# Kernel tuning notes

Measured on AMD Instinct MI355X. Metric: run time of the kernel, lower is better.

## Reference

```python
import jax, jax.numpy as jnp
import numpy as np

HIDDEN = 2048
NUM_HEADS = 16
HEAD_DIM = 128
KV_C = 512
Q_C = 1536
ROPE_DIM = 64
B, S = 2, 2048


def _rope(x):
    # x: [B, H, S, D] with D even; interleaved-pair rotation as in the torch module
    b, h, s, d = x.shape
    inv_freq = 1.0 / (10000.0 ** (jnp.arange(0, d, 2, dtype=jnp.float32) / d))  # [d/2]
    pos = jnp.arange(s, dtype=jnp.float32)
    sinusoid = pos[:, None] * inv_freq[None, :]  # [S, d/2]
    sin, cos = jnp.sin(sinusoid), jnp.cos(sinusoid)
    xr = x.reshape(b, h, s, d // 2, 2)
    x1, x2 = xr[..., 0], xr[..., 1]
    out = jnp.stack([x1 * cos - x2 * sin, x1 * sin + x2 * cos], axis=-1)
    return out.reshape(b, h, s, d)


def setup_inputs() -> dict:
    key = jax.random.key(0)
    ks = jax.random.split(key, 12)

    def lin(k, fan_in, fan_out):
        k1, k2 = jax.random.split(k)
        lim = 1.0 / np.sqrt(fan_in)
        w = jax.random.uniform(k1, (fan_in, fan_out), jnp.float32, -lim, lim)
        b = jax.random.uniform(k2, (fan_out,), jnp.float32, -lim, lim)
        return w, b

    kv_down_w, kv_down_b = lin(ks[0], HIDDEN, KV_C)
    key_up_w, key_up_b = lin(ks[1], KV_C, NUM_HEADS * HEAD_DIM)
    value_up_w, value_up_b = lin(ks[2], KV_C, NUM_HEADS * HEAD_DIM)
    key_rope_w, key_rope_b = lin(ks[3], KV_C, NUM_HEADS * ROPE_DIM)
    query_down_w, query_down_b = lin(ks[4], HIDDEN, Q_C)
    query_up_w, query_up_b = lin(ks[5], Q_C, NUM_HEADS * HEAD_DIM)
    query_rope_w, query_rope_b = lin(ks[6], Q_C, NUM_HEADS * ROPE_DIM)
    out_w, out_b = lin(ks[7], NUM_HEADS * HEAD_DIM, HIDDEN)

    x = jax.random.normal(ks[8], (B, S, HIDDEN), jnp.float32)
    attention_mask = jnp.ones((B, S), dtype=jnp.bool_)  # all tokens valid

    return dict(x=x, attention_mask=attention_mask,
                kv_down_w=kv_down_w, kv_down_b=kv_down_b,
                key_up_w=key_up_w, key_up_b=key_up_b,
                value_up_w=value_up_w, value_up_b=value_up_b,
                key_rope_w=key_rope_w, key_rope_b=key_rope_b,
                query_down_w=query_down_w, query_down_b=query_down_b,
                query_up_w=query_up_w, query_up_b=query_up_b,
                query_rope_w=query_rope_w, query_rope_b=query_rope_b,
                out_w=out_w, out_b=out_b)


def reference(x, attention_mask,
              kv_down_w, kv_down_b, key_up_w, key_up_b,
              value_up_w, value_up_b, key_rope_w, key_rope_b,
              query_down_w, query_down_b, query_up_w, query_up_b,
              query_rope_w, query_rope_b, out_w, out_b):
    b, s, _ = x.shape

    kv_c = x @ kv_down_w + kv_down_b                                 # [B,S,KV_C]
    keys_c = (kv_c @ key_up_w + key_up_b).reshape(b, s, NUM_HEADS, HEAD_DIM).transpose(0, 2, 1, 3)
    values = (kv_c @ value_up_w + value_up_b).reshape(b, s, NUM_HEADS, HEAD_DIM).transpose(0, 2, 1, 3)
    keys_r = (kv_c @ key_rope_w + key_rope_b).reshape(b, s, NUM_HEADS, ROPE_DIM).transpose(0, 2, 1, 3)
    keys_r = _rope(keys_r)

    q_c = x @ query_down_w + query_down_b                            # [B,S,Q_C]
    queries_c = (q_c @ query_up_w + query_up_b).reshape(b, s, NUM_HEADS, HEAD_DIM).transpose(0, 2, 1, 3)
    queries_r = (q_c @ query_rope_w + query_rope_b).reshape(b, s, NUM_HEADS, ROPE_DIM).transpose(0, 2, 1, 3)
    queries_r = _rope(queries_r)

    queries = jnp.concatenate([queries_c, queries_r], axis=-1)      # [B,H,S,HD+RD]
    keys = jnp.concatenate([keys_c, keys_r], axis=-1)

    scale = 1.0 / np.sqrt(HEAD_DIM + ROPE_DIM)
    scores = jnp.einsum('bhqd,bhkd->bhqk', queries, keys) * scale   # [B,H,S,S]

    causal = jnp.triu(jnp.ones((s, s), dtype=jnp.bool_), k=1)       # True = masked
    pad = ~attention_mask                                            # [B,S], True = masked key
    mask = causal[None, None, :, :] | pad[:, None, None, :]
    scores = jnp.where(mask, jnp.float32(-1e9), scores)

    probs = jax.nn.softmax(scores, axis=-1)
    context = jnp.einsum('bhqk,bhkd->bhqd', probs, values)          # [B,H,S,HD]
    context = context.transpose(0, 2, 1, 3).reshape(b, s, NUM_HEADS * HEAD_DIM)
    return context @ out_w + out_b                                   # [B,S,HIDDEN]
```

## Files before the change

kernel.cpp:

```cpp
#include <hip/hip_runtime.h>

typedef unsigned short u16;
typedef short short8 __attribute__((ext_vector_type(8)));
typedef short short4v __attribute__((ext_vector_type(4)));
typedef float floatx4 __attribute__((ext_vector_type(4)));
typedef float floatx4v __attribute__((ext_vector_type(4)));

#define SQ 2048
#define NH 16
#define HD 128
#define RD 64
#define NB 2
#define LDKV 5120
#define LDQ 3072

#define LKC 136
#define LKR 72
#define LVT 72
#define LP  72

#define OFF_BC   ((size_t)0)
#define OFF_WT1  ((size_t)16384)
#define OFF_WT2  (OFF_WT1 + (size_t)2048 * 2048)
#define OFF_WT3  (OFF_WT2 + (size_t)5120 * 512)
#define OFF_WTO  (OFF_WT3 + (size_t)3072 * 1536)
#define OFF_KVQD (OFF_WTO + (size_t)2048 * 2048)
#define OFF_KV   (OFF_KVQD + (size_t)4096 * 2048)
#define OFF_QB   (OFF_KV + (size_t)4096 * 5120)
#define OFF_ROPE (OFF_QB + (size_t)4096 * 3072)

__device__ __forceinline__ float bf2f(u16 u) {
  union { unsigned u; float f; } v; v.u = ((unsigned)u) << 16; return v.f;
}
__device__ __forceinline__ u16 f2bf(float f) {
  union { float f; unsigned u; } v; v.f = f;
  return (u16)((v.u + 0x7FFFu + ((v.u >> 16) & 1u)) >> 16);
}
__device__ __forceinline__ void gll16(const u16* g, u16* l) {
  __builtin_amdgcn_global_load_lds((const __attribute__((address_space(1))) void*)g,
                                   (__attribute__((address_space(3))) void*)l, 16, 0, 0);
}

__global__ __launch_bounds__(256) void prep(
    const float* __restrict__ x,
    const float* b0, const float* b1, const float* b2, const float* b3,
    const float* b4, const float* b5, const float* b6, const float* b7,
    const float* w0, const float* w1, const float* w2, const float* w3,
    const float* w4, const float* w5, const float* w6, const float* w7,
    u16* __restrict__ ws) {
  __shared__ u16 tile[32][33];
  const int blk = blockIdx.x, t = threadIdx.x;

  if (blk < 8192) {
    const int i = blk * 256 + t;
    const floatx4v v = *(const floatx4v*)(x + 4 * (size_t)i);
    short4v o;
    o.x = (short)f2bf(v.x); o.y = (short)f2bf(v.y);
    o.z = (short)f2bf(v.z); o.w = (short)f2bf(v.w);
    *(short4v*)(ws + OFF_QB + 4 * (size_t)i) = o;
    return;
  }
  if (blk < 8240) {
    const int i = (blk - 8192) * 256 + t;
    if (i >= 12288) return;
    float v;
    if      (i < 512)   v = b0[i];
    else if (i < 2048)  v = b1[i - 512];
    else if (i < 4096)  v = b2[i - 2048];
    else if (i < 6144)  v = b3[i - 4096];
    else if (i < 7168)  v = b4[i - 6144];
    else if (i < 9216)  v = b5[i - 7168];
    else if (i < 10240) v = b6[i - 9216];
    else                v = b7[i - 10240];
    ws[OFF_BC + i] = f2bf(v);
    return;
  }
  if (blk >= 23600) {
    const int i = (blk - 23600) * 256 + t;
    const int s = i >> 5, j = i & 31;
    const float inv = exp2f(-(float)j * 0.41524101186092031f);
    float sn, cs;
    sincosf((float)s * inv, &sn, &cs);
    float* rt = (float*)(ws + OFF_ROPE);
    rt[2 * i]     = cs;
    rt[2 * i + 1] = sn;
    return;
  }
  const int f = blk - 8240;
  const float* in; size_t oo; int R, C, start;
  if      (f < 1024)  { in = w0; oo = OFF_WT1;                        R = 2048; C = 512;  start = 0; }
  else if (f < 4096)  { in = w1; oo = OFF_WT1 + (size_t)512 * 2048;   R = 2048; C = 1536; start = 1024; }
  else if (f < 5120)  { in = w2; oo = OFF_WT2;                        R = 512;  C = 2048; start = 4096; }
  else if (f < 6144)  { in = w3; oo = OFF_WT2 + (size_t)2048 * 512;   R = 512;  C = 2048; start = 5120; }
  else if (f < 6656)  { in = w4; oo = OFF_WT2 + (size_t)4096 * 512;   R = 512;  C = 1024; start = 6144; }
  else if (f < 9728)  { in = w5; oo = OFF_WT3;                        R = 1536; C = 2048; start = 6656; }
  else if (f < 11264) { in = w6; oo = OFF_WT3 + (size_t)2048 * 1536;  R = 1536; C = 1024; start = 9728; }
  else                { in = w7; oo = OFF_WTO;                        R = 2048; C = 2048; start = 11264; }
  u16* out = ws + oo;
  const int local = f - start, nx = C / 32;
  const int c0 = (local % nx) * 32, r0 = (local / nx) * 32;
  const int xx = t & 31, y = t >> 5;
#pragma unroll
  for (int i = 0; i < 32; i += 8)
    tile[y + i][xx] = f2bf(in[(size_t)(r0 + y + i) * C + c0 + xx]);
  __syncthreads();
#pragma unroll
  for (int i = 0; i < 32; i += 8)
    out[(size_t)(c0 + y + i) * R + r0 + xx] = tile[xx][y + i];
}

__global__ __launch_bounds__(256) void post(u16* __restrict__ ws) {
  __shared__ u16 tile[32][33];
  const int blk = blockIdx.x, t = threadIdx.x;

  if (blk < 8192) {
    u16* buf = ws + OFF_KV;
    const float* rt = (const float*)(ws + OFF_ROPE);
    const int i = blk * 256 + t;
    const int j = i & 31;
    const int hh = (i >> 5) & 15;
    const int row = i >> 9;
    const int s = row & (SQ - 1);
    u16* p = buf + (size_t)row * LDKV + 4096 + hh * RD + 2 * j;
    const float2 t2 = *(const float2*)(rt + ((size_t)s * 32 + j) * 2);
    const float x1 = bf2f(p[0]), x2 = bf2f(p[1]);
    p[0] = f2bf(x1 * t2.x - x2 * t2.y);
    p[1] = f2bf(x1 * t2.y + x2 * t2.x);
    return;
  }
  const int f = blk - 8192;
  const int bh = f >> 8, rem = f & 255;
  const int b = bh >> 4, hh = bh & 15;
  const int s0 = (rem & 63) * 32, d0 = (rem >> 6) * 32;
  const u16* pin = ws + OFF_KV + (size_t)b * SQ * LDKV + 2048 + (size_t)hh * HD;
  u16* pout = ws + OFF_KVQD + (size_t)bh * HD * SQ;
  const int xx = t & 31, y = t >> 5;
#pragma unroll
  for (int i = 0; i < 32; i += 8)
    tile[y + i][xx] = pin[(size_t)(s0 + y + i) * LDKV + d0 + xx];
  __syncthreads();
#pragma unroll
  for (int i = 0; i < 32; i += 8)
    pout[(size_t)(d0 + y + i) * SQ + s0 + xx] = tile[xx][y + i];
}

__global__ __launch_bounds__(512, 4) void gemm_bt(
    int split,
    const u16* __restrict__ A1, int lda1, const u16* __restrict__ B1,
    const u16* __restrict__ bias1, void* __restrict__ C1, int ldc1, int wf1, int N1, int K1,
    const u16* __restrict__ A2, int lda2, const u16* __restrict__ B2,
    const u16* __restrict__ bias2, void* __restrict__ C2, int ldc2, int wf2, int N2, int K2) {
  __shared__ __align__(16) u16 lAk0[128 * 32];
  __shared__ __align__(16) u16 lAk1[128 * 32];
  __shared__ __align__(16) u16 lBk0[128 * 32];
  __shared__ __align__(16) u16 lBk1[128 * 32];
  int id = blockIdx.x;
  const u16 *A, *Bt, *bias; void* Cout; int lda, ldc, wf32, N, K;
  if (id < split) {
    A = A1; lda = lda1; Bt = B1; bias = bias1; Cout = C1; ldc = ldc1; wf32 = wf1; N = N1; K = K1;
  } else {
    id -= split;
    A = A2; lda = lda2; Bt = B2; bias = bias2; Cout = C2; ldc = ldc2; wf32 = wf2; N = N2; K = K2;
  }
  const int nx = N >> 7;
  const int m0 = (id / nx) * 128, n0 = (id % nx) * 128;
  const int t = threadIdx.x;
  const int lane = t & 63, w = t >> 6;
  const int wm = w & 1, wn = w >> 1;
  const int srow = t >> 2, scol = (t & 3) * 8;
  const u16* gA = A + (size_t)(m0 + srow) * lda + scol;
  const u16* gB = Bt + (size_t)(n0 + srow) * K + scol;
  u16* const ldA0 = lAk0 + (16 * w) * 32;
  u16* const ldA1 = lAk1 + (16 * w) * 32;
  u16* const ldB0 = lBk0 + (16 * w) * 32;
  u16* const ldB1 = lBk1 + (16 * w) * 32;
  const int lane_m = lane & 15, lane_k = (lane >> 4) * 8;
  floatx4 acc[4][2] = {};
  for (int k0 = 0; k0 < K; k0 += 64) {
    gll16(gA + k0, ldA0);
    gll16(gA + k0 + 32, ldA1);
    gll16(gB + k0, ldB0);
    gll16(gB + k0 + 32, ldB1);
    __syncthreads();
    {
      short8 af[4], bf[2];
#pragma unroll
      for (int i = 0; i < 4; i++)
        af[i] = *(const short8*)(lAk0 + (wm * 64 + i * 16 + lane_m) * 32 + lane_k);
#pragma unroll
      for (int i = 0; i < 2; i++)
        bf[i] = *(const short8*)(lBk0 + (wn * 32 + i * 16 + lane_m) * 32 + lane_k);
#pragma unroll
      for (int mi = 0; mi < 4; mi++)
#pragma unroll
        for (int ni = 0; ni < 2; ni++)
          acc[mi][ni] = __builtin_amdgcn_mfma_f32_16x16x32_bf16(af[mi], bf[ni], acc[mi][ni], 0, 0, 0);
    }
    {
      short8 af[4], bf[2];
#pragma unroll
      for (int i = 0; i < 4; i++)
        af[i] = *(const short8*)(lAk1 + (wm * 64 + i * 16 + lane_m) * 32 + lane_k);
#pragma unroll
      for (int i = 0; i < 2; i++)
        bf[i] = *(const short8*)(lBk1 + (wn * 32 + i * 16 + lane_m) * 32 + lane_k);
#pragma unroll
      for (int mi = 0; mi < 4; mi++)
#pragma unroll
        for (int ni = 0; ni < 2; ni++)
          acc[mi][ni] = __builtin_amdgcn_mfma_f32_16x16x32_bf16(af[mi], bf[ni], acc[mi][ni], 0, 0, 0);
    }
    __syncthreads();
  }
  const int quad = lane >> 4;
#pragma unroll
  for (int ni = 0; ni < 2; ni++) {
    const int col = n0 + wn * 32 + ni * 16 + lane_m;
    const float bv = bf2f(bias[col]);
#pragma unroll
    for (int mi = 0; mi < 4; mi++) {
      const int row = m0 + wm * 64 + mi * 16 + quad * 4;
      if (wf32) {
        float* pc = (float*)Cout + (size_t)row * ldc + col;
#pragma unroll
        for (int r = 0; r < 4; r++)
          pc[(size_t)r * ldc] = acc[mi][ni][r] + bv;
      } else {
        u16* pc = (u16*)Cout + (size_t)row * ldc + col;
#pragma unroll
        for (int r = 0; r < 4; r++)
          pc[(size_t)r * ldc] = f2bf(acc[mi][ni][r] + bv);
      }
    }
  }
}

__global__ __launch_bounds__(512, 4) void flash_attn(const u16* __restrict__ Q,
                                                     const u16* __restrict__ KV,
                                                     const u16* __restrict__ Vt,
                                                     const float* __restrict__ rt,
                                                     u16* __restrict__ Ctx) {
  __shared__ __align__(16) u16 lKc[64 * LKC];
  __shared__ __align__(16) u16 lKr[64 * LKR];
  __shared__ __align__(16) u16 lVt[128 * LVT];
  __shared__ __align__(16) u16 lP[8 * 16 * LP];
  const int t = threadIdx.x, lane = t & 63, w = t >> 6;
  const int col = blockIdx.y;
  const int qtile = (col < 16) ? (15 - (int)blockIdx.x) : (int)blockIdx.x;
  const int h = col & (NH - 1);
  const int b = col >> 4;
  const int q0 = qtile * 128;
  const int nkt = 2 * qtile + 2;
  const int lane_m = lane & 15, quad = lane >> 4, lane_k = quad * 8;

  const int qrow = q0 + 16 * w + lane_m;
  const u16* qcp = Q + (size_t)(b * SQ + qrow) * LDQ + h * HD;
  const u16* qrp = Q + (size_t)(b * SQ + qrow) * LDQ + 2048 + h * RD;
  short8 qfc[4], qfr[2];
#pragma unroll
  for (int ks = 0; ks < 4; ks++) qfc[ks] = *(const short8*)(qcp + ks * 32 + lane_k);
  {
#pragma unroll
    for (int ks = 0; ks < 2; ks++) {
      short8 v = *(const short8*)(qrp + ks * 32 + lane_k);
#pragma unroll
      for (int p = 0; p < 4; p++) {
        const int j = ks * 16 + quad * 4 + p;
        const float2 t2 = *(const float2*)(rt + ((size_t)qrow * 32 + j) * 2);
        const float x1 = bf2f((u16)v[2 * p]), x2 = bf2f((u16)v[2 * p + 1]);
        v[2 * p]     = (short)f2bf(x1 * t2.x - x2 * t2.y);
        v[2 * p + 1] = (short)f2bf(x1 * t2.y + x2 * t2.x);
      }
      qfr[ks] = v;
    }
  }

  floatx4 O[8] = {};
  float mrow[4], lsum[4];
#pragma unroll
  for (int r = 0; r < 4; r++) { mrow[r] = -1e30f; lsum[r] = 0.f; }

  const u16* gKc = KV + (size_t)b * SQ * LDKV + h * HD;
  const u16* gKr = KV + (size_t)b * SQ * LDKV + 4096 + h * RD;
  const u16* gVt = Vt + (size_t)(b * NH + h) * HD * SQ;
  const float C2 = 0.10412825525540364f;
  const float THR = 28.8f;

  short8 rKc[2], rKr, rVt[2];
  auto load_tile = [&](int kb) {
#pragma unroll
    for (int i = 0; i < 2; i++) {
      const int c = t + i * 512, row = c >> 4, cc = (c & 15) * 8;
      rKc[i] = *(const short8*)(gKc + (size_t)(kb + row) * LDKV + cc);
    }
    {
      const int row = t >> 3, cc = (t & 7) * 8;
      rKr = *(const short8*)(gKr + (size_t)(kb + row) * LDKV + cc);
    }
#pragma unroll
    for (int i = 0; i < 2; i++) {
      const int c = t + i * 512, row = c >> 3, cc = (c & 7) * 8;
      rVt[i] = *(const short8*)(gVt + (size_t)row * SQ + kb + cc);
    }
  };

  const int wrow_lo = q0 + 16 * w;
  const int wrow_hi = wrow_lo + 15;

  load_tile(0);
  for (int kt = 0; kt < nkt; kt++) {
    const int kb = kt * 64;
    __syncthreads();
#pragma unroll
    for (int i = 0; i < 2; i++) {
      const int c = t + i * 512, row = c >> 4, cc = (c & 15) * 8;
      *(short8*)(lKc + row * LKC + cc) = rKc[i];
    }
    {
      const int row = t >> 3, cc = (t & 7) * 8;
      *(short8*)(lKr + row * LKR + cc) = rKr;
    }
#pragma unroll
    for (int i = 0; i < 2; i++) {
      const int c = t + i * 512, row = c >> 3, cc = (c & 7) * 8;
      *(short8*)(lVt + row * LVT + cc) = rVt[i];
    }
    __syncthreads();
    if (kt < nkt - 1) load_tile(kb + 64);

    if (kb <= wrow_hi) {
      float ss[4][4];
      __builtin_amdgcn_s_setprio(1);
#pragma unroll
      for (int n = 0; n < 4; n++) {
        floatx4 a = {0.f, 0.f, 0.f, 0.f};
#pragma unroll
        for (int ks = 0; ks < 4; ks++) {
          const short8 kf = *(const short8*)(lKc + (n * 16 + lane_m) * LKC + ks * 32 + lane_k);
          a = __builtin_amdgcn_mfma_f32_16x16x32_bf16(qfc[ks], kf, a, 0, 0, 0);
        }
#pragma unroll
        for (int ks = 0; ks < 2; ks++) {
          const short8 kf = *(const short8*)(lKr + (n * 16 + lane_m) * LKR + ks * 32 + lane_k);
          a = __builtin_amdgcn_mfma_f32_16x16x32_bf16(qfr[ks], kf, a, 0, 0, 0);
        }
#pragma unroll
        for (int r = 0; r < 4; r++) ss[n][r] = a[r];
      }
      __builtin_amdgcn_s_setprio(0);
      if (kb + 63 > wrow_lo) {
#pragma unroll
        for (int n = 0; n < 4; n++) {
          const int kcol = kb + n * 16 + lane_m;
#pragma unroll
          for (int r = 0; r < 4; r++) {
            const int row = wrow_lo + quad * 4 + r;
            if (kcol > row) ss[n][r] = -1e30f;
          }
        }
      }
      float mt[4];
#pragma unroll
      for (int r = 0; r < 4; r++) {
        float m = fmaxf(fmaxf(ss[0][r], ss[1][r]), fmaxf(ss[2][r], ss[3][r]));
#pragma unroll
        for (int d = 1; d < 16; d <<= 1) m = fmaxf(m, __shfl_xor(m, d));
        mt[r] = m;
      }
      const bool grow = (mt[0] > mrow[0] + THR) || (mt[1] > mrow[1] + THR) ||
                        (mt[2] > mrow[2] + THR) || (mt[3] > mrow[3] + THR);
      if (__any(grow)) {
#pragma unroll
        for (int r = 0; r < 4; r++) {
          const float mn = fmaxf(mrow[r], mt[r]);
          const float alpha = exp2f((mrow[r] - mn) * C2);
          mrow[r] = mn;
          lsum[r] *= alpha;
#pragma unroll
          for (int vb = 0; vb < 8; vb++) O[vb][r] *= alpha;
        }
      }
      float pw[4][4];
#pragma unroll
      for (int r = 0; r < 4; r++) {
        float s = 0.f;
#pragma unroll
        for (int n = 0; n < 4; n++) {
          const float p = exp2f((ss[n][r] - mrow[r]) * C2);
          pw[n][r] = p;
          s += p;
        }
#pragma unroll
        for (int d = 1; d < 16; d <<= 1) s += __shfl_xor(s, d);
        lsum[r] += s;
      }
#pragma unroll
      for (int n = 0; n < 4; n++)
#pragma unroll
        for (int r = 0; r < 4; r++)
          lP[(w * 16 + quad * 4 + r) * LP + n * 16 + lane_m] = f2bf(pw[n][r]);
      asm volatile("s_waitcnt lgkmcnt(0)" ::: "memory");
      __builtin_amdgcn_s_setprio(1);
#pragma unroll
      for (int ks = 0; ks < 2; ks++) {
        const short8 pf = *(const short8*)(lP + (w * 16 + lane_m) * LP + ks * 32 + lane_k);
#pragma unroll
        for (int vb = 0; vb < 8; vb++) {
          const short8 vf = *(const short8*)(lVt + (vb * 16 + lane_m) * LVT + ks * 32 + lane_k);
          O[vb] = __builtin_amdgcn_mfma_f32_16x16x32_bf16(pf, vf, O[vb], 0, 0, 0);
        }
      }
      __builtin_amdgcn_s_setprio(0);
    }
  }
  float inv[4];
#pragma unroll
  for (int r = 0; r < 4; r++) inv[r] = 1.f / lsum[r];
#pragma unroll
  for (int vb = 0; vb < 8; vb++) {
#pragma unroll
    for (int r = 0; r < 4; r++) {
      const int row = wrow_lo + quad * 4 + r;
      Ctx[(size_t)(b * SQ + row) * 2048 + h * HD + vb * 16 + lane_m] = f2bf(O[vb][r] * inv[r]);
    }
  }
}

extern "C" void kernel_launch(void* const* d_in, const int* in_sizes, int n_in,
                              void* d_out, int out_size, void* d_ws, size_t ws_size,
                              hipStream_t stream) {
  (void)in_sizes; (void)n_in; (void)out_size; (void)ws_size;
  const float* x    = (const float*)d_in[0];
  const float* kvdw = (const float*)d_in[2];
  const float* kvdb = (const float*)d_in[3];
  const float* kuw  = (const float*)d_in[4];
  const float* kub  = (const float*)d_in[5];
  const float* vuw  = (const float*)d_in[6];
  const float* vub  = (const float*)d_in[7];
  const float* krw  = (const float*)d_in[8];
  const float* krb  = (const float*)d_in[9];
  const float* qdw  = (const float*)d_in[10];
  const float* qdb  = (const float*)d_in[11];
  const float* quw  = (const float*)d_in[12];
  const float* qub  = (const float*)d_in[13];
  const float* qrw  = (const float*)d_in[14];
  const float* qrb  = (const float*)d_in[15];
  const float* ow   = (const float*)d_in[16];
  const float* ob   = (const float*)d_in[17];

  u16* ws   = (u16*)d_ws;
  u16* bc   = ws + OFF_BC;
  u16* WT1  = ws + OFF_WT1;
  u16* WT2  = ws + OFF_WT2;
  u16* WT3  = ws + OFF_WT3;
  u16* WTo  = ws + OFF_WTO;
  u16* KVQd = ws + OFF_KVQD;
  u16* KV   = ws + OFF_KV;
  u16* Qb   = ws + OFF_QB;
  const float* rt = (const float*)(ws + OFF_ROPE);
  u16* Ctx  = WT1;
  u16* Vt   = KVQd;
  u16* xc   = Qb;
  const u16* nu = (const u16*)nullptr;

  prep<<<dim3(23856), 256, 0, stream>>>(x, kvdb, qdb, kub, vub, krb, qub, qrb, ob,
                                        kvdw, qdw, kuw, vuw, krw, quw, qrw, ow, ws);

  gemm_bt<<<dim3(512), 512, 0, stream>>>(1 << 30,
      xc, 2048, WT1, bc, KVQd, 2048, 0, 2048, 2048,
      nu, 0, nu, nu, (void*)nullptr, 0, 0, 0, 64);

  gemm_bt<<<dim3(2048), 512, 0, stream>>>(1280,
      KVQd, 2048, WT2, bc + 2048, KV, LDKV, 0, 5120, 512,
      KVQd + 512, 2048, WT3, bc + 7168, Qb, LDQ, 0, 3072, 1536);

  post<<<dim3(16384), 256, 0, stream>>>(ws);

  flash_attn<<<dim3(16, 32), 512, 0, stream>>>(Qb, KV, Vt, rt, Ctx);

  gemm_bt<<<dim3(512), 512, 0, stream>>>(1 << 30,
      Ctx, 2048, WTo, bc + 10240, d_out, 2048, 1, 2048, 2048,
      nu, 0, nu, nu, (void*)nullptr, 0, 0, 0, 64);
}
```

Before: 496.8 us.

## Fuse key RoPE and V transpose into the up-projection GEMM epilogue

The post kernel used to apply RoPE to the key-rope columns and transpose V for flash attention in a separate pass. The KV up-projection GEMM now does both in its epilogue. It rotates rope columns using a lane shuffle to fetch the pair partner, and writes V straight in transposed layout to a new workspace region. This removes one full kernel launch and its read/write traffic over KV, but only when the workspace is large enough. Otherwise it falls back to a standalone transpose kernel, and the scattered transposed stores (4 elements per store) may be less coalesced.

New measurement: 476.9 us. 4.0% less time.

```diff
diff --git a/kernel.cpp b/kernel.cpp
--- a/kernel.cpp
+++ b/kernel.cpp
@@ -28,6 +28,8 @@
 #define OFF_KV   (OFF_KVQD + (size_t)4096 * 2048)
 #define OFF_QB   (OFF_KV + (size_t)4096 * 5120)
 #define OFF_ROPE (OFF_QB + (size_t)4096 * 3072)
+#define OFF_VT   (OFF_ROPE + (size_t)262144)
+#define WS_NEED_BIG ((OFF_VT + (size_t)32 * 128 * 2048) * 2)
 
 __device__ __forceinline__ float bf2f(u16 u) {
   union { unsigned u; float f; } v; v.u = ((unsigned)u) << 16; return v.f;
@@ -109,26 +111,9 @@
     out[(size_t)(c0 + y + i) * R + r0 + xx] = tile[xx][y + i];
 }
 
-__global__ __launch_bounds__(256) void post(u16* __restrict__ ws) {
+__global__ __launch_bounds__(256) void transpose_v(u16* __restrict__ ws) {
   __shared__ u16 tile[32][33];
-  const int blk = blockIdx.x, t = threadIdx.x;
-
-  if (blk < 8192) {
-    u16* buf = ws + OFF_KV;
-    const float* rt = (const float*)(ws + OFF_ROPE);
-    const int i = blk * 256 + t;
-    const int j = i & 31;
-    const int hh = (i >> 5) & 15;
-    const int row = i >> 9;
-    const int s = row & (SQ - 1);
-    u16* p = buf + (size_t)row * LDKV + 4096 + hh * RD + 2 * j;
-    const float2 t2 = *(const float2*)(rt + ((size_t)s * 32 + j) * 2);
-    const float x1 = bf2f(p[0]), x2 = bf2f(p[1]);
-    p[0] = f2bf(x1 * t2.x - x2 * t2.y);
-    p[1] = f2bf(x1 * t2.y + x2 * t2.x);
-    return;
-  }
-  const int f = blk - 8192;
+  const int f = blockIdx.x, t = threadIdx.x;
   const int bh = f >> 8, rem = f & 255;
   const int b = bh >> 4, hh = bh & 15;
   const int s0 = (rem & 63) * 32, d0 = (rem >> 6) * 32;
@@ -145,22 +130,22 @@
 }
 
 __global__ __launch_bounds__(512, 4) void gemm_bt(
-    int split,
+    int split, const float* __restrict__ rt, u16* __restrict__ vt,
     const u16* __restrict__ A1, int lda1, const u16* __restrict__ B1,
-    const u16* __restrict__ bias1, void* __restrict__ C1, int ldc1, int wf1, int N1, int K1,
+    const u16* __restrict__ bias1, void* __restrict__ C1, int ldc1, int m1, int N1, int K1,
     const u16* __restrict__ A2, int lda2, const u16* __restrict__ B2,
-    const u16* __restrict__ bias2, void* __restrict__ C2, int ldc2, int wf2, int N2, int K2) {
+    const u16* __restrict__ bias2, void* __restrict__ C2, int ldc2, int m2, int N2, int K2) {
   __shared__ __align__(16) u16 lAk0[128 * 32];
   __shared__ __align__(16) u16 lAk1[128 * 32];
   __shared__ __align__(16) u16 lBk0[128 * 32];
   __shared__ __align__(16) u16 lBk1[128 * 32];
   int id = blockIdx.x;
-  const u16 *A, *Bt, *bias; void* Cout; int lda, ldc, wf32, N, K;
+  const u16 *A, *Bt, *bias; void* Cout; int lda, ldc, mode, N, K;
   if (id < split) {
-    A = A1; lda = lda1; Bt = B1; bias = bias1; Cout = C1; ldc = ldc1; wf32 = wf1; N = N1; K = K1;
+    A = A1; lda = lda1; Bt = B1; bias = bias1; Cout = C1; ldc = ldc1; mode = m1; N = N1; K = K1;
   } else {
     id -= split;
-    A = A2; lda = lda2; Bt = B2; bias = bias2; Cout = C2; ldc = ldc2; wf32 = wf2; N = N2; K = K2;
+    A = A2; lda = lda2; Bt = B2; bias = bias2; Cout = C2; ldc = ldc2; mode = m2; N = N2; K = K2;
   }
   const int nx = N >> 7;
   const int m0 = (id / nx) * 128, n0 = (id % nx) * 128;
@@ -213,6 +198,49 @@
     __syncthreads();
   }
   const int quad = lane >> 4;
+
+  if (mode == 2 && n0 >= 2048 && n0 < 4096 && vt) {
+#pragma unroll
+    for (int ni = 0; ni < 2; ni++) {
+      const int col = n0 + wn * 32 + ni * 16 + lane_m;
+      const float bv = bf2f(bias[col]);
+      const int hh = (col - 2048) >> 7, d = (col - 2048) & 127;
+#pragma unroll
+      for (int mi = 0; mi < 4; mi++) {
+        const int row = m0 + wm * 64 + mi * 16 + quad * 4;
+        const int b = row >> 11, s0v = row & 2047;
+        short4v o;
+#pragma unroll
+        for (int r = 0; r < 4; r++) o[r] = (short)f2bf(acc[mi][ni][r] + bv);
+        *(short4v*)(vt + ((size_t)(b * 16 + hh) * 128 + d) * 2048 + s0v) = o;
+      }
+    }
+    return;
+  }
+  if (mode == 2 && n0 >= 4096) {
+#pragma unroll
+    for (int ni = 0; ni < 2; ni++) {
+      const int col = n0 + wn * 32 + ni * 16 + lane_m;
+      const float bv = bf2f(bias[col]);
+      const int j = ((col - 4096) & 63) >> 1;
+      const bool even = !(col & 1);
+      u16* pc = (u16*)Cout + (size_t)(m0 + wm * 64) * ldc + col;
+#pragma unroll
+      for (int mi = 0; mi < 4; mi++) {
+        const int row = m0 + wm * 64 + mi * 16 + quad * 4;
+#pragma unroll
+        for (int r = 0; r < 4; r++) {
+          const int s = (row + r) & 2047;
+          const float val = acc[mi][ni][r] + bv;
+          const float par = __shfl_xor(val, 1);
+          const float2 t2 = *(const float2*)(rt + ((size_t)s * 32 + j) * 2);
+          const float out = even ? val * t2.x - par * t2.y : val * t2.x + par * t2.y;
+          pc[(size_t)(mi * 16 + quad * 4 + r) * ldc] = f2bf(out);
+        }
+      }
+    }
+    return;
+  }
 #pragma unroll
   for (int ni = 0; ni < 2; ni++) {
     const int col = n0 + wn * 32 + ni * 16 + lane_m;
@@ -220,7 +248,7 @@
 #pragma unroll
     for (int mi = 0; mi < 4; mi++) {
       const int row = m0 + wm * 64 + mi * 16 + quad * 4;
-      if (wf32) {
+      if (mode == 1) {
         float* pc = (float*)Cout + (size_t)row * ldc + col;
 #pragma unroll
         for (int r = 0; r < 4; r++)
@@ -429,7 +457,7 @@
 extern "C" void kernel_launch(void* const* d_in, const int* in_sizes, int n_in,
                               void* d_out, int out_size, void* d_ws, size_t ws_size,
                               hipStream_t stream) {
-  (void)in_sizes; (void)n_in; (void)out_size; (void)ws_size;
+  (void)in_sizes; (void)n_in; (void)out_size;
   const float* x    = (const float*)d_in[0];
   const float* kvdw = (const float*)d_in[2];
   const float* kvdb = (const float*)d_in[3];
@@ -459,26 +487,30 @@
   u16* Qb   = ws + OFF_QB;
   const float* rt = (const float*)(ws + OFF_ROPE);
   u16* Ctx  = WT1;
-  u16* Vt   = KVQd;
   u16* xc   = Qb;
   const u16* nu = (const u16*)nullptr;
 
+  const bool big = ws_size >= WS_NEED_BIG;
+  u16* Vt     = big ? (ws + OFF_VT) : KVQd;
+  u16* vt_arg = big ? (ws + OFF_VT) : (u16*)nullptr;
+
   prep<<<dim3(23856), 256, 0, stream>>>(x, kvdb, qdb, kub, vub, krb, qub, qrb, ob,
                                         kvdw, qdw, kuw, vuw, krw, quw, qrw, ow, ws);
 
-  gemm_bt<<<dim3(512), 512, 0, stream>>>(1 << 30,
+  gemm_bt<<<dim3(512), 512, 0, stream>>>(1 << 30, rt, (u16*)nullptr,
       xc, 2048, WT1, bc, KVQd, 2048, 0, 2048, 2048,
       nu, 0, nu, nu, (void*)nullptr, 0, 0, 0, 64);
 
-  gemm_bt<<<dim3(2048), 512, 0, stream>>>(1280,
-      KVQd, 2048, WT2, bc + 2048, KV, LDKV, 0, 5120, 512,
+  gemm_bt<<<dim3(2048), 512, 0, stream>>>(1280, rt, vt_arg,
+      KVQd, 2048, WT2, bc + 2048, KV, LDKV, 2, 5120, 512,
       KVQd + 512, 2048, WT3, bc + 7168, Qb, LDQ, 0, 3072, 1536);
 
-  post<<<dim3(16384), 256, 0, stream>>>(ws);
+  if (!big)
+    transpose_v<<<dim3(8192), 256, 0, stream>>>(ws);
 
   flash_attn<<<dim3(16, 32), 512, 0, stream>>>(Qb, KV, Vt, rt, Ctx);
 
-  gemm_bt<<<dim3(512), 512, 0, stream>>>(1 << 30,
+  gemm_bt<<<dim3(512), 512, 0, stream>>>(1 << 30, rt, (u16*)nullptr,
       Ctx, 2048, WTo, bc + 10240, d_out, 2048, 1, 2048, 2048,
       nu, 0, nu, nu, (void*)nullptr, 0, 0, 0, 64);
 }
```
